# Kernel optimization log

Hardware: AMD Instinct MI355X
Metric: run time of the kernel (lower is better)

The kernel has to match this reference:

```python
import jax, jax.numpy as jnp
import numpy as np

B, S, D = 4, 1024, 1024   # batch, seq_len, d_model (isize=hsize=osize)
H, AD = 16, 64            # num_head, attn_dim = hsize // num_head
K_REL = 16                # k_rel_pos (bidirectional: 2*K+1 = 33 embeddings)
EPS = 1e-8                # SparseNormer eps (ieps_default)


def setup_inputs() -> dict:
    key = jax.random.key(0)
    ks = jax.random.split(key, 5)
    scale = 0.02
    return {
        "iQ": jax.random.normal(ks[0], (B, S, D), jnp.float32),
        "Wa": jax.random.normal(ks[1], (3 * D, D), jnp.float32) * scale,   # adaptor weight
        "ba": jnp.zeros((3 * D,), jnp.float32),                            # adaptor bias
        "rel_emb": jax.random.normal(ks[2], (2 * K_REL + 1, AD), jnp.float32) * scale,
        "sn_bias": jnp.zeros((1,), jnp.float32),                           # SparseNormer bias
        "Wo": jax.random.normal(ks[3], (D, D), jnp.float32) * scale,       # outer weight
        "bo": jnp.zeros((D,), jnp.float32),                                # outer bias
    }


def reference(iQ, Wa, ba, rel_emb, sn_bias, Wo, bo):
    b, s, _ = iQ.shape
    # fused QKV projection: [B,S,3*H*AD] -> q,k,v each [B,H,S,AD]
    qkv = (iQ @ Wa.T + ba).reshape(b, s, 3, H, AD)
    q = qkv[:, :, 0].transpose(0, 2, 1, 3)
    k = qkv[:, :, 1].transpose(0, 2, 1, 3)
    v = qkv[:, :, 2].transpose(0, 2, 1, 3)

    # content scores [B,H,S,S]
    scores = jnp.einsum('bhqd,bhkd->bhqk', q, k)

    # relative-position term: rel_pos[i,j] = clip(j-i, -K, K) + K
    pos = jnp.arange(s)
    rp = jnp.clip(pos[None, :] - pos[:, None], -K_REL, K_REL) + K_REL  # [S,S] int
    r = rel_emb[rp]                                                     # [S,S,AD]
    scores = scores + jnp.einsum('bhqd,qkd->bhqk', q, r)

    scores = scores / jnp.sqrt(jnp.asarray(AD, scores.dtype))

    # SparseNormer: relu(x + b)^2 / (sum + eps)
    t = jax.nn.relu(scores + sn_bias)
    t = t * t
    attn = t / (t.sum(-1, keepdims=True) + EPS)

    ctx = jnp.einsum('bhqk,bhkd->bhqd', attn, v)          # [B,H,S,AD]
    ctx = ctx.transpose(0, 2, 1, 3).reshape(b, s, H * AD)  # [B,S,hsize]
    return ctx @ Wo.T + bo
```

## Files before the change

kernel.cpp:

```cpp
#include <hip/hip_runtime.h>
#include <hip/hip_bf16.h>
#include <stdint.h>

typedef unsigned short u16;
typedef unsigned int   u32;
typedef __attribute__((ext_vector_type(8))) __bf16 bf16x8;
typedef __attribute__((ext_vector_type(4))) float  f32x4;
typedef __attribute__((ext_vector_type(2))) u32    u32x2;
typedef __attribute__((ext_vector_type(4))) u32    u32x4;

#define B_  4
#define S_  1024
#define D_  1024
#define H_  16
#define AD_ 64

#if defined(__has_builtin)
#if __has_builtin(__builtin_amdgcn_cvt_pk_bf16_f32)
#define HAVE_CVT_PK 1
#endif
#if __has_builtin(__builtin_amdgcn_global_load_lds)
#define HAVE_GLL 1
#endif
#endif

#ifdef HAVE_CVT_PK
typedef __attribute__((ext_vector_type(2))) __bf16 bf16x2;
__device__ __forceinline__ u32 pack2(float a, float b) {
    bf16x2 r = __builtin_amdgcn_cvt_pk_bf16_f32(a, b);
    return __builtin_bit_cast(u32, r);
}
__device__ __forceinline__ u16 f2bf(float f) { return (u16)pack2(f, f); }
#else
__device__ __forceinline__ u16 f2bf(float f) {
    u32 u = __float_as_uint(f);
    u32 r = u + 0x7fffu + ((u >> 16) & 1u);
    return (u16)(r >> 16);
}
__device__ __forceinline__ u32 pack2(float a, float b) {
    return (u32)f2bf(a) | ((u32)f2bf(b) << 16);
}
#endif

typedef __attribute__((address_space(1))) const u32 gas_u32;
typedef __attribute__((address_space(3))) u32 las_u32;
__device__ __forceinline__ void gll16(const void* g, void* l) {
#ifdef HAVE_GLL
    __builtin_amdgcn_global_load_lds((gas_u32*)g, (las_u32*)l, 16, 0, 0);
#else
    int lane = threadIdx.x & 63;
    *(uint4*)((u16*)l + lane * 8) = *(const uint4*)g;
#endif
}

__global__ __launch_bounds__(256) void conv_bf16(
    const float* __restrict__ a, const float* __restrict__ b,
    const float* __restrict__ c,
    u16* __restrict__ ao, u16* __restrict__ bo, u16* __restrict__ co,
    int na, int nb)
{
    int gid = blockIdx.x * 256 + threadIdx.x;
    int base = gid * 8;
    const float* src; u16* dst; int off;
    if (base < na)           { src = a; dst = ao; off = base; }
    else if (base < na + nb) { src = b; dst = bo; off = base - na; }
    else                     { src = c; dst = co; off = base - na - nb; }
    float4 v0 = *(const float4*)(src + off);
    float4 v1 = *(const float4*)(src + off + 4);
    u32 pk[4] = {pack2(v0.x, v0.y), pack2(v0.z, v0.w),
                 pack2(v1.x, v1.y), pack2(v1.z, v1.w)};
    *(uint4*)(dst + off) = *(uint4*)pk;
}

__global__ __launch_bounds__(256, 3) void qkv_gemm(
    const u16* __restrict__ A, const u16* __restrict__ W,
    const float* __restrict__ bias,
    u16* __restrict__ qb, u16* __restrict__ kb, u16* __restrict__ vb)
{
    __shared__ u16 As[128 * 64];
    __shared__ u16 Bs[128 * 64];

    const int tid  = threadIdx.x;
    const int lane = tid & 63, w = tid >> 6;
    const int quad = lane >> 4, ln = lane & 15;
    const int wrow = (w >> 1) * 64, wcol = (w & 1) * 64;
    const int row0 = blockIdx.y * 128, col0 = blockIdx.x * 128;

    const int ri = lane >> 3, ci = lane & 7;
    const int scol = (ci ^ ri) << 3;

    f32x4 acc[4][4];
#pragma unroll
    for (int i = 0; i < 4; i++)
#pragma unroll
        for (int j = 0; j < 4; j++) acc[i][j] = (f32x4){0.f, 0.f, 0.f, 0.f};

    for (int kb_i = 0; kb_i < 16; ++kb_i) {
        const int k0 = kb_i * 64;
#pragma unroll
        for (int c = 0; c < 4; ++c) {
            int r0 = c * 32 + w * 8;
            int gr = r0 + ri;
            gll16(A + (size_t)(row0 + gr) * D_ + k0 + scol, &As[r0 * 64]);
            gll16(W + (size_t)(col0 + gr) * D_ + k0 + scol, &Bs[r0 * 64]);
        }
        __syncthreads();
#pragma unroll
        for (int ks = 0; ks < 2; ++ks) {
            bf16x8 af[4], bfr[4];
#pragma unroll
            for (int mt = 0; mt < 4; ++mt) {
                int r = wrow + mt * 16 + ln;
                af[mt] = *(bf16x8*)&As[r * 64 + (((ks * 4 + quad) ^ (r & 7)) << 3)];
            }
#pragma unroll
            for (int nt = 0; nt < 4; ++nt) {
                int r = wcol + nt * 16 + ln;
                bfr[nt] = *(bf16x8*)&Bs[r * 64 + (((ks * 4 + quad) ^ (r & 7)) << 3)];
            }
#pragma unroll
            for (int mt = 0; mt < 4; ++mt)
#pragma unroll
                for (int nt = 0; nt < 4; ++nt)
                    acc[mt][nt] = __builtin_amdgcn_mfma_f32_16x16x32_bf16(
                        af[mt], bfr[nt], acc[mt][nt], 0, 0, 0);
        }
        __syncthreads();
    }

    const int which = col0 >> 10;
#pragma unroll
    for (int mt = 0; mt < 4; ++mt) {
#pragma unroll
        for (int nt = 0; nt < 4; ++nt) {
            int n = col0 + wcol + nt * 16 + ln;
            float bv = bias[n];
            int h = (n >> 6) & 15, d = n & 63;
            if (which == 2) {
                int m0 = row0 + wrow + mt * 16 + quad * 4;
                int b = m0 >> 10, s0 = m0 & 1023;
                u32x2 pk;
                pk.x = pack2(acc[mt][nt][0] + bv, acc[mt][nt][1] + bv);
                pk.y = pack2(acc[mt][nt][2] + bv, acc[mt][nt][3] + bv);
                *(u32x2*)&vb[((size_t)((b * 16 + h) * 64 + d)) * 1024 + s0] = pk;
            } else {
#pragma unroll
                for (int reg = 0; reg < 4; ++reg) {
                    int m = row0 + wrow + mt * 16 + quad * 4 + reg;
                    int b = m >> 10, s = m & 1023;
                    float v = acc[mt][nt][reg] + bv;
                    if (which == 0)
                        qb[((size_t)((b * 16 + h) * 1024 + s)) * 64 + d] = f2bf(v * 0.125f);
                    else
                        kb[((size_t)((b * 16 + h) * 1024 + s)) * 64 + d] = f2bf(v);
                }
            }
        }
    }
}

__global__ __launch_bounds__(256) void attn_kernel(
    const u16* __restrict__ qb, const u16* __restrict__ kb,
    const u16* __restrict__ vb, const float* __restrict__ rel,
    const float* __restrict__ snb_p, u16* __restrict__ ctx)
{
    __shared__ u16 q_s[128 * 64];
    __shared__ u16 k_s[2][64 * 64];
    __shared__ u16 v_s[2][64 * 64];
    __shared__ float qr[33 * 128];

    u16* t_s   = q_s;
    u16* rel_s = v_s[1];

    const int tid  = threadIdx.x;
    const int lane = tid & 63, w = tid >> 6;
    const int quad = lane >> 4, ln = lane & 15;
    const int bh = blockIdx.x >> 3, qt = blockIdx.x & 7;
    const int i0 = qt * 128;
    const float snb = snb_p[0];

    const u16* qplane = qb + ((size_t)bh * 1024 + i0) * 64;
    const u16* kplane = kb + (size_t)bh * 1024 * 64;
    const u16* vplane = vb + (size_t)bh * 64 * 1024;

    const int ri = lane >> 3, ci = lane & 7;
    const int scol = (ci ^ ri) << 3;

    const u32x4 ones_u = {0x3F803F80u, 0x3F803F80u, 0x3F803F80u, 0x3F803F80u};
    const bf16x8 ones = __builtin_bit_cast(bf16x8, ones_u);

#pragma unroll
    for (int c = 0; c < 4; ++c) {
        int r0 = w * 32 + c * 8;
        gll16(qplane + (size_t)(r0 + ri) * 64 + scol, &q_s[r0 * 64]);
    }
    for (int idx = tid; idx < 384; idx += 256) {
        int p = idx >> 3, c = idx & 7;
        u32 pk[4];
        if (p < 33) {
            const float* sp = rel + p * 64 + c * 8;
            float4 r0 = *(const float4*)sp;
            float4 r1 = *(const float4*)(sp + 4);
            pk[0] = pack2(r0.x, r0.y); pk[1] = pack2(r0.z, r0.w);
            pk[2] = pack2(r1.x, r1.y); pk[3] = pack2(r1.z, r1.w);
        } else { pk[0] = pk[1] = pk[2] = pk[3] = 0; }
        *(uint4*)&rel_s[p * 64 + ((c ^ (p & 7)) << 3)] = *(uint4*)pk;
    }
    __syncthreads();

    bf16x8 bq[2][2];
#pragma unroll
    for (int sub = 0; sub < 2; ++sub) {
        int rq = w * 32 + sub * 16 + ln;
#pragma unroll
        for (int ks = 0; ks < 2; ++ks)
            bq[sub][ks] = *(bf16x8*)&q_s[rq * 64 + (((ks * 4 + quad) ^ (rq & 7)) << 3)];
    }

#pragma unroll
    for (int sub = 0; sub < 2; ++sub) {
        f32x4 qacc[3];
#pragma unroll
        for (int nt = 0; nt < 3; ++nt) qacc[nt] = (f32x4){0.f, 0.f, 0.f, 0.f};
#pragma unroll
        for (int ks = 0; ks < 2; ++ks) {
#pragma unroll
            for (int nt = 0; nt < 3; ++nt) {
                int rp = nt * 16 + ln;
                bf16x8 bp = *(bf16x8*)&rel_s[rp * 64 + (((ks * 4 + quad) ^ (rp & 7)) << 3)];
                qacc[nt] = __builtin_amdgcn_mfma_f32_16x16x32_bf16(bq[sub][ks], bp, qacc[nt], 0, 0, 0);
            }
        }
#pragma unroll
        for (int nt = 0; nt < 3; ++nt) {
            int p = nt * 16 + ln;
            if (p < 33) {
#pragma unroll
                for (int reg = 0; reg < 4; ++reg)
                    qr[p * 128 + w * 32 + sub * 16 + quad * 4 + reg] = qacc[nt][reg] + snb;
            }
        }
    }

#pragma unroll
    for (int c = 0; c < 2; ++c) {
        int r0 = w * 16 + c * 8;
        gll16(kplane + (size_t)(r0 + ri) * 64 + scol, &k_s[0][r0 * 64]);
        gll16(vplane + (size_t)(r0 + ri) * 1024 + scol, &v_s[0][r0 * 64]);
    }
    __syncthreads();

    float cL[2], cR[2];
#pragma unroll
    for (int sub = 0; sub < 2; ++sub) {
        int il = w * 32 + sub * 16 + ln;
        cL[sub] = qr[il];
        cR[sub] = qr[32 * 128 + il];
    }

    f32x4 o_acc[2][4], lacc[2];
#pragma unroll
    for (int sub = 0; sub < 2; ++sub) {
        lacc[sub] = (f32x4){0.f, 0.f, 0.f, 0.f};
#pragma unroll
        for (int nt = 0; nt < 4; ++nt) o_acc[sub][nt] = (f32x4){0.f, 0.f, 0.f, 0.f};
    }

    for (int jt = 0; jt < 16; ++jt) {
        const int cur = jt & 1;
        const int j0 = jt * 64;
        if (jt < 15) {
            const int nxt = 1 - cur;
#pragma unroll
            for (int c = 0; c < 2; ++c) {
                int r0 = w * 16 + c * 8;
                gll16(kplane + (size_t)(j0 + 64 + r0 + ri) * 64 + scol, &k_s[nxt][r0 * 64]);
                gll16(vplane + (size_t)(r0 + ri) * 1024 + (j0 + 64) + scol, &v_s[nxt][r0 * 64]);
            }
        }

        f32x4 sacc[2][4];
#pragma unroll
        for (int sub = 0; sub < 2; ++sub)
#pragma unroll
            for (int mj = 0; mj < 4; ++mj) sacc[sub][mj] = (f32x4){0.f, 0.f, 0.f, 0.f};
#pragma unroll
        for (int ks = 0; ks < 2; ++ks) {
#pragma unroll
            for (int mj = 0; mj < 4; ++mj) {
                int rk = mj * 16 + ln;
                bf16x8 ak = *(bf16x8*)&k_s[cur][rk * 64 + (((ks * 4 + quad) ^ (rk & 7)) << 3)];
                sacc[0][mj] = __builtin_amdgcn_mfma_f32_16x16x32_bf16(ak, bq[0][ks], sacc[0][mj], 0, 0, 0);
                sacc[1][mj] = __builtin_amdgcn_mfma_f32_16x16x32_bf16(ak, bq[1][ks], sacc[1][mj], 0, 0, 0);
            }
        }

#pragma unroll
        for (int sub = 0; sub < 2; ++sub) {
            const int ib = i0 + w * 32 + sub * 16;
            const int row = w * 32 + sub * 16 + ln;
#pragma unroll
            for (int mj = 0; mj < 4; ++mj) {
                const int jg0 = j0 + mj * 16;
                const int diff = jg0 - ib;
                float tv[4];
                if (diff >= 32 || diff <= -32) {
                    const float c = (diff < 0) ? cL[sub] : cR[sub];
#pragma unroll
                    for (int reg = 0; reg < 4; ++reg) {
                        float t = fmaxf(sacc[sub][mj][reg] + c, 0.f);
                        tv[reg] = t * t;
                    }
                } else {
#pragma unroll
                    for (int reg = 0; reg < 4; ++reg) {
                        int dlt = jg0 + quad * 4 + reg - (ib + ln);
                        int p = min(max(dlt, -16), 16) + 16;
                        float t = fmaxf(sacc[sub][mj][reg] + qr[p * 128 + row], 0.f);
                        tv[reg] = t * t;
                    }
                }
                u32x2 pk;
                pk.x = pack2(tv[0], tv[1]);
                pk.y = pack2(tv[2], tv[3]);
                int chunk = ((2 * mj + (quad >> 1)) ^ (row & 7));
                *(u32x2*)&t_s[row * 64 + (chunk << 3) + (quad & 1) * 4] = pk;
            }
        }

#pragma unroll
        for (int ks = 0; ks < 2; ++ks) {
            bf16x8 at[2];
#pragma unroll
            for (int sub = 0; sub < 2; ++sub) {
                int rt = w * 32 + sub * 16 + ln;
                at[sub] = *(bf16x8*)&t_s[rt * 64 + (((ks * 4 + quad) ^ (rt & 7)) << 3)];
            }
            lacc[0] = __builtin_amdgcn_mfma_f32_16x16x32_bf16(at[0], ones, lacc[0], 0, 0, 0);
            lacc[1] = __builtin_amdgcn_mfma_f32_16x16x32_bf16(at[1], ones, lacc[1], 0, 0, 0);
#pragma unroll
            for (int nt = 0; nt < 4; ++nt) {
                int rv = nt * 16 + ln;
                bf16x8 bv = *(bf16x8*)&v_s[cur][rv * 64 + (((ks * 4 + quad) ^ (rv & 7)) << 3)];
                o_acc[0][nt] = __builtin_amdgcn_mfma_f32_16x16x32_bf16(at[0], bv, o_acc[0][nt], 0, 0, 0);
                o_acc[1][nt] = __builtin_amdgcn_mfma_f32_16x16x32_bf16(at[1], bv, o_acc[1][nt], 0, 0, 0);
            }
        }
        __syncthreads();
    }

    const int b = bh >> 4, h = bh & 15;
#pragma unroll
    for (int sub = 0; sub < 2; ++sub) {
#pragma unroll
        for (int reg = 0; reg < 4; ++reg) {
            int ig = i0 + w * 32 + sub * 16 + quad * 4 + reg;
            float li = 1.f / (lacc[sub][reg] + 1e-8f);
#pragma unroll
            for (int nt = 0; nt < 4; ++nt) {
                int dg = nt * 16 + ln;
                ctx[((size_t)(b * 1024 + ig)) * 1024 + h * 64 + dg] =
                    f2bf(o_acc[sub][nt][reg] * li);
            }
        }
    }
}

__global__ __launch_bounds__(256) void out_gemm(
    const u16* __restrict__ A, const u16* __restrict__ W,
    const float* __restrict__ bias, float* __restrict__ out)
{
    __shared__ u16 As[128 * 128];
    __shared__ u16 Bs[64 * 128];

    const int tid  = threadIdx.x;
    const int lane = tid & 63, w = tid >> 6;
    const int quad = lane >> 4, ln = lane & 15;
    const int wrow = (w >> 1) * 64, wcol = (w & 1) * 32;
    const int row0 = blockIdx.y * 128, col0 = blockIdx.x * 64;

    const int ri4  = lane >> 4;
    const int ci16 = lane & 15;

    f32x4 acc[4][2];
#pragma unroll
    for (int i = 0; i < 4; i++)
#pragma unroll
        for (int j = 0; j < 2; j++) acc[i][j] = (f32x4){0.f, 0.f, 0.f, 0.f};

    for (int kb_i = 0; kb_i < 8; ++kb_i) {
        const int k0 = kb_i * 128;
#pragma unroll
        for (int c = 0; c < 8; ++c) {
            int r0 = c * 16 + w * 4;
            int r = r0 + ri4;
            int sc = (ci16 ^ (r & 7)) << 3;
            gll16(A + (size_t)(row0 + r) * D_ + k0 + sc, &As[r0 * 128]);
        }
#pragma unroll
        for (int c = 0; c < 4; ++c) {
            int r0 = c * 16 + w * 4;
            int r = r0 + ri4;
            int sc = (ci16 ^ (r & 7)) << 3;
            gll16(W + (size_t)(col0 + r) * D_ + k0 + sc, &Bs[r0 * 128]);
        }
        __syncthreads();
#pragma unroll
        for (int ks = 0; ks < 4; ++ks) {
            bf16x8 af[4], bfr[2];
#pragma unroll
            for (int mt = 0; mt < 4; ++mt) {
                int r = wrow + mt * 16 + ln;
                af[mt] = *(bf16x8*)&As[r * 128 + (((ks * 4 + quad) ^ (r & 7)) << 3)];
            }
#pragma unroll
            for (int nt = 0; nt < 2; ++nt) {
                int r = wcol + nt * 16 + ln;
                bfr[nt] = *(bf16x8*)&Bs[r * 128 + (((ks * 4 + quad) ^ (r & 7)) << 3)];
            }
#pragma unroll
            for (int mt = 0; mt < 4; ++mt)
#pragma unroll
                for (int nt = 0; nt < 2; ++nt)
                    acc[mt][nt] = __builtin_amdgcn_mfma_f32_16x16x32_bf16(
                        af[mt], bfr[nt], acc[mt][nt], 0, 0, 0);
        }
        __syncthreads();
    }
#pragma unroll
    for (int mt = 0; mt < 4; ++mt) {
#pragma unroll
        for (int nt = 0; nt < 2; ++nt) {
            int n = col0 + wcol + nt * 16 + ln;
            float bv = bias[n];
#pragma unroll
            for (int reg = 0; reg < 4; ++reg) {
                int m = row0 + wrow + mt * 16 + quad * 4 + reg;
                out[(size_t)m * D_ + n] = acc[mt][nt][reg] + bv;
            }
        }
    }
}

extern "C" void kernel_launch(void* const* d_in, const int* in_sizes, int n_in,
                              void* d_out, int out_size, void* d_ws, size_t ws_size,
                              hipStream_t stream)
{
    const float* iQ  = (const float*)d_in[0];
    const float* Wa  = (const float*)d_in[1];
    const float* ba  = (const float*)d_in[2];
    const float* rel = (const float*)d_in[3];
    const float* snb = (const float*)d_in[4];
    const float* Wo  = (const float*)d_in[5];
    const float* bo  = (const float*)d_in[6];
    float* outp = (float*)d_out;

    const size_t NQ = (size_t)B_ * S_ * D_;
    const size_t NWA = (size_t)3 * D_ * D_;
    const size_t NWO = (size_t)D_ * D_;
    const size_t PLANE = (size_t)B_ * H_ * S_ * AD_;

    u16* iQbf = (u16*)d_ws;
    u16* Wabf = iQbf + NQ;
    u16* Wobf = Wabf + NWA;
    u16* qbuf = Wobf + NWO;
    u16* kbuf = qbuf + PLANE;
    u16* vbuf = kbuf + PLANE;
    u16* ctx  = iQbf;

    conv_bf16<<<4096, 256, 0, stream>>>(iQ, Wa, Wo, iQbf, Wabf, Wobf,
                                        (int)NQ, (int)NWA);
    qkv_gemm<<<dim3(24, 32), 256, 0, stream>>>(iQbf, Wabf, ba, qbuf, kbuf, vbuf);
    attn_kernel<<<dim3(512), 256, 0, stream>>>(qbuf, kbuf, vbuf, rel, snb, ctx);
    out_gemm<<<dim3(16, 32), 256, 0, stream>>>(ctx, Wobf, bo, outp);
}
```

Baseline: 175.6 us.

## Halve attention query tile to 64 rows and fold far rel-pos bias into MFMA init

```diff
diff --git a/kernel.cpp b/kernel.cpp
--- a/kernel.cpp
+++ b/kernel.cpp
@@ -164,25 +164,24 @@
     const u16* __restrict__ vb, const float* __restrict__ rel,
     const float* __restrict__ snb_p, u16* __restrict__ ctx)
 {
-    __shared__ u16 q_s[128 * 64];
+    __shared__ u16 q_s[64 * 64];
     __shared__ u16 k_s[2][64 * 64];
     __shared__ u16 v_s[2][64 * 64];
-    __shared__ float qr[33 * 128];
-
-    u16* t_s   = q_s;
+    __shared__ float qr[33 * 64];
+    u16* t_s = q_s;
     u16* rel_s = v_s[1];
 
     const int tid  = threadIdx.x;
     const int lane = tid & 63, w = tid >> 6;
     const int quad = lane >> 4, ln = lane & 15;
-    const int bh = blockIdx.x >> 3, qt = blockIdx.x & 7;
-    const int i0 = qt * 128;
+    const int strip = w * 16;
+    const int bh = blockIdx.x >> 4, qt = blockIdx.x & 15;
+    const int i0 = qt * 64;
     const float snb = snb_p[0];
 
     const u16* qplane = qb + ((size_t)bh * 1024 + i0) * 64;
     const u16* kplane = kb + (size_t)bh * 1024 * 64;
     const u16* vplane = vb + (size_t)bh * 64 * 1024;
-
     const int ri = lane >> 3, ci = lane & 7;
     const int scol = (ci ^ ri) << 3;
 
@@ -190,8 +189,8 @@
     const bf16x8 ones = __builtin_bit_cast(bf16x8, ones_u);
 
 #pragma unroll
-    for (int c = 0; c < 4; ++c) {
-        int r0 = w * 32 + c * 8;
+    for (int c = 0; c < 2; ++c) {
+        int r0 = strip + c * 8;
         gll16(qplane + (size_t)(r0 + ri) * 64 + scol, &q_s[r0 * 64]);
     }
     for (int idx = tid; idx < 384; idx += 256) {
@@ -208,17 +207,13 @@
     }
     __syncthreads();
 
-    bf16x8 bq[2][2];
-#pragma unroll
-    for (int sub = 0; sub < 2; ++sub) {
-        int rq = w * 32 + sub * 16 + ln;
-#pragma unroll
-        for (int ks = 0; ks < 2; ++ks)
-            bq[sub][ks] = *(bf16x8*)&q_s[rq * 64 + (((ks * 4 + quad) ^ (rq & 7)) << 3)];
-    }
-
-#pragma unroll
-    for (int sub = 0; sub < 2; ++sub) {
+    const int iloc = strip + ln;
+    bf16x8 bq[2];
+#pragma unroll
+    for (int ks = 0; ks < 2; ++ks)
+        bq[ks] = *(bf16x8*)&q_s[iloc * 64 + (((ks * 4 + quad) ^ (iloc & 7)) << 3)];
+
+    {
         f32x4 qacc[3];
 #pragma unroll
         for (int nt = 0; nt < 3; ++nt) qacc[nt] = (f32x4){0.f, 0.f, 0.f, 0.f};
@@ -228,7 +223,7 @@
             for (int nt = 0; nt < 3; ++nt) {
                 int rp = nt * 16 + ln;
                 bf16x8 bp = *(bf16x8*)&rel_s[rp * 64 + (((ks * 4 + quad) ^ (rp & 7)) << 3)];
-                qacc[nt] = __builtin_amdgcn_mfma_f32_16x16x32_bf16(bq[sub][ks], bp, qacc[nt], 0, 0, 0);
+                qacc[nt] = __builtin_amdgcn_mfma_f32_16x16x32_bf16(bq[ks], bp, qacc[nt], 0, 0, 0);
             }
         }
 #pragma unroll
@@ -237,113 +232,95 @@
             if (p < 33) {
 #pragma unroll
                 for (int reg = 0; reg < 4; ++reg)
-                    qr[p * 128 + w * 32 + sub * 16 + quad * 4 + reg] = qacc[nt][reg] + snb;
-            }
-        }
-    }
-
+                    qr[p * 64 + strip + quad * 4 + reg] = qacc[nt][reg] + snb;
+            }
+        }
+    }
 #pragma unroll
     for (int c = 0; c < 2; ++c) {
-        int r0 = w * 16 + c * 8;
+        int r0 = strip + c * 8;
         gll16(kplane + (size_t)(r0 + ri) * 64 + scol, &k_s[0][r0 * 64]);
         gll16(vplane + (size_t)(r0 + ri) * 1024 + scol, &v_s[0][r0 * 64]);
     }
     __syncthreads();
 
-    float cL[2], cR[2];
-#pragma unroll
-    for (int sub = 0; sub < 2; ++sub) {
-        int il = w * 32 + sub * 16 + ln;
-        cL[sub] = qr[il];
-        cR[sub] = qr[32 * 128 + il];
-    }
-
-    f32x4 o_acc[2][4], lacc[2];
-#pragma unroll
-    for (int sub = 0; sub < 2; ++sub) {
-        lacc[sub] = (f32x4){0.f, 0.f, 0.f, 0.f};
-#pragma unroll
-        for (int nt = 0; nt < 4; ++nt) o_acc[sub][nt] = (f32x4){0.f, 0.f, 0.f, 0.f};
-    }
-
+    const float cL = qr[iloc];
+    const float cR = qr[32 * 64 + iloc];
+
+    f32x4 o_acc[4], lacc = (f32x4){0.f, 0.f, 0.f, 0.f};
+#pragma unroll
+    for (int nt = 0; nt < 4; ++nt) o_acc[nt] = (f32x4){0.f, 0.f, 0.f, 0.f};
+
+    const int ib = i0 + strip;
     for (int jt = 0; jt < 16; ++jt) {
-        const int cur = jt & 1;
         const int j0 = jt * 64;
+        u16* kc = k_s[jt & 1];
+        u16* vc = v_s[jt & 1];
         if (jt < 15) {
-            const int nxt = 1 - cur;
+            u16* kn = k_s[1 - (jt & 1)];
+            u16* vn = v_s[1 - (jt & 1)];
 #pragma unroll
             for (int c = 0; c < 2; ++c) {
-                int r0 = w * 16 + c * 8;
-                gll16(kplane + (size_t)(j0 + 64 + r0 + ri) * 64 + scol, &k_s[nxt][r0 * 64]);
-                gll16(vplane + (size_t)(r0 + ri) * 1024 + (j0 + 64) + scol, &v_s[nxt][r0 * 64]);
-            }
-        }
-
-        f32x4 sacc[2][4];
-#pragma unroll
-        for (int sub = 0; sub < 2; ++sub)
-#pragma unroll
-            for (int mj = 0; mj < 4; ++mj) sacc[sub][mj] = (f32x4){0.f, 0.f, 0.f, 0.f};
+                int r0 = strip + c * 8;
+                gll16(kplane + (size_t)(j0 + 64 + r0 + ri) * 64 + scol, &kn[r0 * 64]);
+                gll16(vplane + (size_t)(r0 + ri) * 1024 + (j0 + 64) + scol, &vn[r0 * 64]);
+            }
+        }
+
+        f32x4 sacc[4];
+        bool faru[4];
+#pragma unroll
+        for (int mj = 0; mj < 4; ++mj) {
+            const int diff = (j0 + mj * 16) - ib;
+            faru[mj] = (diff >= 32 || diff <= -32);
+            float ci = faru[mj] ? ((diff < 0) ? cL : cR) : 0.f;
+            sacc[mj] = (f32x4){ci, ci, ci, ci};
+        }
 #pragma unroll
         for (int ks = 0; ks < 2; ++ks) {
 #pragma unroll
             for (int mj = 0; mj < 4; ++mj) {
                 int rk = mj * 16 + ln;
-                bf16x8 ak = *(bf16x8*)&k_s[cur][rk * 64 + (((ks * 4 + quad) ^ (rk & 7)) << 3)];
-                sacc[0][mj] = __builtin_amdgcn_mfma_f32_16x16x32_bf16(ak, bq[0][ks], sacc[0][mj], 0, 0, 0);
-                sacc[1][mj] = __builtin_amdgcn_mfma_f32_16x16x32_bf16(ak, bq[1][ks], sacc[1][mj], 0, 0, 0);
-            }
-        }
-
-#pragma unroll
-        for (int sub = 0; sub < 2; ++sub) {
-            const int ib = i0 + w * 32 + sub * 16;
-            const int row = w * 32 + sub * 16 + ln;
-#pragma unroll
-            for (int mj = 0; mj < 4; ++mj) {
-                const int jg0 = j0 + mj * 16;
-                const int diff = jg0 - ib;
-                float tv[4];
-                if (diff >= 32 || diff <= -32) {
-                    const float c = (diff < 0) ? cL[sub] : cR[sub];
-#pragma unroll
-                    for (int reg = 0; reg < 4; ++reg) {
-                        float t = fmaxf(sacc[sub][mj][reg] + c, 0.f);
-                        tv[reg] = t * t;
-                    }
-                } else {
-#pragma unroll
-                    for (int reg = 0; reg < 4; ++reg) {
-                        int dlt = jg0 + quad * 4 + reg - (ib + ln);
-                        int p = min(max(dlt, -16), 16) + 16;
-                        float t = fmaxf(sacc[sub][mj][reg] + qr[p * 128 + row], 0.f);
-                        tv[reg] = t * t;
-                    }
+                bf16x8 ak = *(bf16x8*)&kc[rk * 64 + (((ks * 4 + quad) ^ (rk & 7)) << 3)];
+                sacc[mj] = __builtin_amdgcn_mfma_f32_16x16x32_bf16(ak, bq[ks], sacc[mj], 0, 0, 0);
+            }
+        }
+
+#pragma unroll
+        for (int mj = 0; mj < 4; ++mj) {
+            const int jg0 = j0 + mj * 16;
+            float tv[4];
+            if (faru[mj]) {
+#pragma unroll
+                for (int reg = 0; reg < 4; ++reg) {
+                    float t = fmaxf(sacc[mj][reg], 0.f);
+                    tv[reg] = t * t;
                 }
-                u32x2 pk;
-                pk.x = pack2(tv[0], tv[1]);
-                pk.y = pack2(tv[2], tv[3]);
-                int chunk = ((2 * mj + (quad >> 1)) ^ (row & 7));
-                *(u32x2*)&t_s[row * 64 + (chunk << 3) + (quad & 1) * 4] = pk;
-            }
+            } else {
+#pragma unroll
+                for (int reg = 0; reg < 4; ++reg) {
+                    int dlt = jg0 + quad * 4 + reg - (ib + ln);
+                    int p = min(max(dlt, -16), 16) + 16;
+                    float t = fmaxf(sacc[mj][reg] + qr[p * 64 + iloc], 0.f);
+                    tv[reg] = t * t;
+                }
+            }
+            u32x2 pk;
+            pk.x = pack2(tv[0], tv[1]);
+            pk.y = pack2(tv[2], tv[3]);
+            int chunk = (2 * mj + (quad >> 1)) ^ (iloc & 7);
+            *(u32x2*)&t_s[iloc * 64 + (chunk << 3) + (quad & 1) * 4] = pk;
         }
 
 #pragma unroll
         for (int ks = 0; ks < 2; ++ks) {
-            bf16x8 at[2];
-#pragma unroll
-            for (int sub = 0; sub < 2; ++sub) {
-                int rt = w * 32 + sub * 16 + ln;
-                at[sub] = *(bf16x8*)&t_s[rt * 64 + (((ks * 4 + quad) ^ (rt & 7)) << 3)];
-            }
-            lacc[0] = __builtin_amdgcn_mfma_f32_16x16x32_bf16(at[0], ones, lacc[0], 0, 0, 0);
-            lacc[1] = __builtin_amdgcn_mfma_f32_16x16x32_bf16(at[1], ones, lacc[1], 0, 0, 0);
+            bf16x8 at = *(bf16x8*)&t_s[iloc * 64 + (((ks * 4 + quad) ^ (iloc & 7)) << 3)];
+            lacc = __builtin_amdgcn_mfma_f32_16x16x32_bf16(at, ones, lacc, 0, 0, 0);
 #pragma unroll
             for (int nt = 0; nt < 4; ++nt) {
                 int rv = nt * 16 + ln;
-                bf16x8 bv = *(bf16x8*)&v_s[cur][rv * 64 + (((ks * 4 + quad) ^ (rv & 7)) << 3)];
-                o_acc[0][nt] = __builtin_amdgcn_mfma_f32_16x16x32_bf16(at[0], bv, o_acc[0][nt], 0, 0, 0);
-                o_acc[1][nt] = __builtin_amdgcn_mfma_f32_16x16x32_bf16(at[1], bv, o_acc[1][nt], 0, 0, 0);
+                bf16x8 bv = *(bf16x8*)&vc[rv * 64 + (((ks * 4 + quad) ^ (rv & 7)) << 3)];
+                o_acc[nt] = __builtin_amdgcn_mfma_f32_16x16x32_bf16(at, bv, o_acc[nt], 0, 0, 0);
             }
         }
         __syncthreads();
@@ -351,17 +328,14 @@
 
     const int b = bh >> 4, h = bh & 15;
 #pragma unroll
-    for (int sub = 0; sub < 2; ++sub) {
-#pragma unroll
-        for (int reg = 0; reg < 4; ++reg) {
-            int ig = i0 + w * 32 + sub * 16 + quad * 4 + reg;
-            float li = 1.f / (lacc[sub][reg] + 1e-8f);
-#pragma unroll
-            for (int nt = 0; nt < 4; ++nt) {
-                int dg = nt * 16 + ln;
-                ctx[((size_t)(b * 1024 + ig)) * 1024 + h * 64 + dg] =
-                    f2bf(o_acc[sub][nt][reg] * li);
-            }
+    for (int reg = 0; reg < 4; ++reg) {
+        int ig = i0 + strip + quad * 4 + reg;
+        float li = 1.f / (lacc[reg] + 1e-8f);
+#pragma unroll
+        for (int nt = 0; nt < 4; ++nt) {
+            int dg = nt * 16 + ln;
+            ctx[((size_t)(b * 1024 + ig)) * 1024 + h * 64 + dg] =
+                f2bf(o_acc[nt][reg] * li);
         }
     }
 }
@@ -471,6 +445,6 @@
     conv_bf16<<<4096, 256, 0, stream>>>(iQ, Wa, Wo, iQbf, Wabf, Wobf,
                                         (int)NQ, (int)NWA);
     qkv_gemm<<<dim3(24, 32), 256, 0, stream>>>(iQbf, Wabf, ba, qbuf, kbuf, vbuf);
-    attn_kernel<<<dim3(512), 256, 0, stream>>>(qbuf, kbuf, vbuf, rel, snb, ctx);
+    attn_kernel<<<dim3(1024), 256, 0, stream>>>(qbuf, kbuf, vbuf, rel, snb, ctx);
     out_gemm<<<dim3(16, 32), 256, 0, stream>>>(ctx, Wobf, bo, outp);
 }
```

After: 184.3 us. +5.0%, slower.
